# Kernel optimization log

Measured on AMD Instinct MI355X. Metric: run time of the kernel, lower is better.

## Reference

```python
import jax, jax.numpy as jnp
import numpy as np

B, N, G = 32, 1024, 8   # batch, Nvecs (= k_in), Nglobals
K_OUT, H = 128, 128     # MLP output width, hidden width
D_IN = 1 + N + G        # MLP input width: [u, norm, dots]


def setup_inputs() -> dict:
    key = jax.random.key(0)
    ks = jax.random.split(key, 8)
    x = jax.random.uniform(ks[0], (B, N, 3), dtype=jnp.float32)  # positive coords -> dots >= 0
    u = jax.random.normal(ks[1], (B, G), dtype=jnp.float32)
    s0 = 1.0 / np.sqrt(D_IN)
    s1 = 1.0 / np.sqrt(H)
    W0 = jax.random.normal(ks[2], (D_IN, H), dtype=jnp.float32) * s0
    b0 = jnp.zeros((H,), dtype=jnp.float32)
    W1 = jax.random.normal(ks[3], (H, H), dtype=jnp.float32) * s1
    b1 = jnp.zeros((H,), dtype=jnp.float32)
    W2 = jax.random.normal(ks[4], (H, K_OUT), dtype=jnp.float32) * s1
    b2 = jnp.zeros((K_OUT,), dtype=jnp.float32)
    return {"x": x, "u": u, "W0": W0, "b0": b0, "W1": W1, "b1": b1, "W2": W2, "b2": b2}


def reference(x, u, W0, b0, W1, b1, W2, b2):
    # x: [B, N, 3], u: [B, G]
    norms = jnp.linalg.norm(x, axis=-1, keepdims=True)            # [B, N, 1]
    dots = jnp.sqrt(jnp.einsum('bid,bjd->bij', x, x))             # [B, N, N]
    u_rep = jnp.broadcast_to(u[:, None, :], (x.shape[0], x.shape[1], u.shape[-1]))
    scalars = jnp.concatenate([u_rep, norms, dots], axis=-1)      # [B, N, G+1+N]
    # MLP (Linear -> LeakyReLU -> Linear -> LeakyReLU -> Linear)
    h = jax.nn.leaky_relu(scalars @ W0 + b0)
    h = jax.nn.leaky_relu(h @ W1 + b1)
    fk = h @ W2 + b2                                              # [B, N, K_OUT]
    # outer product 'bio,bid->biod' followed by mean over i == fused contraction
    out = jnp.einsum('bio,bid->bod', fk, x) / x.shape[1]          # [B, K_OUT, 3]
    return out
```

## Files before the change

### kernel.cpp

```cpp
#include <hip/hip_runtime.h>
#include <hip/hip_fp16.h>

typedef _Float16 f16;
typedef f16 f16x4 __attribute__((ext_vector_type(4)));
typedef f16 f16x8 __attribute__((ext_vector_type(8)));
typedef float f32x4 __attribute__((ext_vector_type(4)));

#define NN 1024

#define IMG_OFF   0
#define W8_OFF    327680
#define BIAS0_OFF 328192

__global__ __launch_bounds__(256) void prep_kernel(
    const float* __restrict__ u,  const float* __restrict__ W0,
    const float* __restrict__ b0, const float* __restrict__ W1,
    const float* __restrict__ W2,
    f16* __restrict__ img, float* __restrict__ w8v, float* __restrict__ bias0,
    float* __restrict__ outp)
{
    const int t = threadIdx.x;
    const int blk = blockIdx.x;
    if (blk < 160) {
        int flat = blk * 1024 + t * 4;
        int c = flat >> 13;
        int rem = flat & 8191;
        int r = rem >> 6;
        int s = rem & 63;
        int colb = s ^ ((r & 7) << 3);
        f16x4 v;
#pragma unroll
        for (int e = 0; e < 4; ++e) {
            int col = colb + e;
            float val;
            if (c < 16)       val = W0[(9 + c * 64 + col) * 128 + r];
            else if (c == 16) val = W1[col * 128 + r];
            else if (c == 17) val = W1[(64 + col) * 128 + r];
            else if (c == 18) val = W2[col * 128 + r];
            else              val = W2[(64 + col) * 128 + r];
            v[e] = (f16)val;
        }
        *(f16x4*)&img[flat] = v;
    } else if (blk < 176) {
        int idx = (blk - 160) * 256 + t;
        int b = idx >> 7, h = idx & 127;
        float s = b0[h];
#pragma unroll
        for (int g = 0; g < 8; ++g) s += u[b * 8 + g] * W0[g * 128 + h];
        bias0[idx] = s;
    } else if (blk == 176) {
        if (t < 128) w8v[t] = W0[8 * 128 + t];
    } else {
        int idx = (blk - 177) * 1024 + t * 4;
        if (idx < 12288) { float4 z = {0.f, 0.f, 0.f, 0.f}; *(float4*)&outp[idx] = z; }
    }
}

__global__ __launch_bounds__(256, 3) void fused_kernel(
    const float* __restrict__ x, const float* __restrict__ b1p,
    const float* __restrict__ b2p, const f16* __restrict__ img,
    const float* __restrict__ w8v, const float* __restrict__ bias0,
    float* __restrict__ outp)
{
    __shared__ __align__(16) f16 Dsh[2][64 * 64];
    __shared__ __align__(16) f16 Wsh[2][128 * 64];
    __shared__ __align__(16) float xi[64 * 4];
    __shared__ float normv[64];
    __shared__ float biass[128];
    __shared__ float w8s[128];

    const int t = threadIdx.x;
    const int b = blockIdx.x >> 4;
    const int i0 = (blockIdx.x & 15) * 64;

    if (t < 192) {
        int i = t / 3, d = t - i * 3;
        xi[i * 4 + d] = x[(size_t)(b * NN + i0 + i) * 3 + d];
    }
    if (t < 128) { biass[t] = bias0[b * 128 + t]; w8s[t] = w8v[t]; }
    __syncthreads();
    if (t < 64) {
        float a0 = xi[t * 4], a1 = xi[t * 4 + 1], a2 = xi[t * 4 + 2];
        normv[t] = __builtin_amdgcn_sqrtf(a0 * a0 + a1 * a1 + a2 * a2);
    }

    const int lane = t & 63, wv = t >> 6;
    const int wm = wv >> 1, wn = wv & 1;
    const int lm = lane & 15, q = lane >> 4;

    f16x4 bi[4];
#pragma unroll
    for (int it = 0; it < 4; ++it) {
        f16x4 v; v[0] = (f16)0; v[1] = (f16)0; v[2] = (f16)0; v[3] = (f16)0;
        if (q == 0) {
            int ii = it * 16 + lm;
            v[0] = (f16)xi[ii * 4];
            v[1] = (f16)xi[ii * 4 + 1];
            v[2] = (f16)xi[ii * 4 + 2];
        }
        bi[it] = v;
    }

    f16x4 aj[16];
#pragma unroll
    for (int jc = 0; jc < 16; ++jc) {
        f16x4 a; a[0] = (f16)0; a[1] = (f16)0; a[2] = (f16)0; a[3] = (f16)0;
        if (q == 0) {
            const float* p = x + (size_t)(b * NN + jc * 64 + wv * 16 + lm) * 3;
            a[0] = (f16)p[0]; a[1] = (f16)p[1]; a[2] = (f16)p[2];
        }
        aj[jc] = a;
    }

    f32x4 acc[2][4];
    auto zero_acc = [&]() {
#pragma unroll
        for (int mt = 0; mt < 2; ++mt)
#pragma unroll
            for (int nt = 0; nt < 4; ++nt)
#pragma unroll
                for (int e = 0; e < 4; ++e) acc[mt][nt][e] = 0.f;
    };
    zero_acc();

    auto stage = [&](int c, int buf) {
        const f16* g = img + c * 8192;
#pragma unroll
        for (int k = 0; k < 4; ++k) {
            int off = (t + k * 256) * 8;
            __builtin_amdgcn_global_load_lds(
                (const __attribute__((address_space(1))) unsigned int*)(g + off),
                (__attribute__((address_space(3))) unsigned int*)(&Wsh[buf][off]),
                16, 0, 0);
        }
    };

    auto dotstore = [&](f16x4 ajf, int buf) {
        f32x4 cg[4];
#pragma unroll
        for (int it = 0; it < 4; ++it) {
            f32x4 z; z[0] = 0.f; z[1] = 0.f; z[2] = 0.f; z[3] = 0.f;
            cg[it] = __builtin_amdgcn_mfma_f32_16x16x16f16(ajf, bi[it], z, 0, 0, 0);
        }
#pragma unroll
        for (int it = 0; it < 4; ++it) {
            f16x4 dv;
#pragma unroll
            for (int r = 0; r < 4; ++r)
                dv[r] = (f16)__builtin_amdgcn_sqrtf(fmaxf(cg[it][r], 0.f));
            int row = it * 16 + lm;
            int colstart = wv * 16 + q * 4;
            int addr = row * 64 + (((colstart & ~7) ^ ((row & 7) << 3)) | (colstart & 7));
            *(f16x4*)&Dsh[buf][addr] = dv;
        }
    };

    auto mfma2 = [&](const f16* Ab, const f16* Bb) {
#pragma unroll
        for (int ks = 0; ks < 2; ++ks) {
            const int col = ks * 32 + q * 8;
            f16x8 af[2], bf[4];
#pragma unroll
            for (int mt = 0; mt < 2; ++mt) {
                int row = wm * 32 + mt * 16 + lm;
                af[mt] = *(const f16x8*)(Ab + row * 64 + (col ^ ((row & 7) << 3)));
            }
#pragma unroll
            for (int nt = 0; nt < 4; ++nt) {
                int row = wn * 64 + nt * 16 + lm;
                bf[nt] = *(const f16x8*)(Bb + row * 64 + (col ^ ((row & 7) << 3)));
            }
#pragma unroll
            for (int mt = 0; mt < 2; ++mt)
#pragma unroll
                for (int nt = 0; nt < 4; ++nt)
                    acc[mt][nt] = __builtin_amdgcn_mfma_f32_16x16x32_f16(
                        af[mt], bf[nt], acc[mt][nt], 0, 0, 0);
        }
    };

    stage(0, 0);
    dotstore(aj[0], 0);
    __syncthreads();

#pragma unroll
    for (int jc = 0; jc < 16; ++jc) {
        const int cur = jc & 1, nxt = cur ^ 1;
        stage(jc + 1, nxt);
        if (jc < 15) dotstore(aj[jc + 1], nxt);
        mfma2(Dsh[cur], Wsh[cur]);
        __syncthreads();
    }

#pragma unroll
    for (int mt = 0; mt < 2; ++mt)
#pragma unroll
        for (int nt = 0; nt < 4; ++nt) {
            const int h = wn * 64 + nt * 16 + lm;
            const float bh = biass[h], w8h = w8s[h];
            const int hh = h & 63;
#pragma unroll
            for (int r = 0; r < 4; ++r) {
                int i = wm * 32 + mt * 16 + q * 4 + r;
                float val = acc[mt][nt][r] + bh + normv[i] * w8h;
                val = val > 0.f ? val : 0.01f * val;
                int addr = i * 64 + (((hh & ~7) ^ ((i & 7) << 3)) | (hh & 7));
                Dsh[wn][addr] = (f16)val;
            }
        }
    stage(17, 1);
    __syncthreads();

    zero_acc();
    mfma2(Dsh[0], Wsh[0]);
    mfma2(Dsh[1], Wsh[1]);
    __syncthreads();

#pragma unroll
    for (int mt = 0; mt < 2; ++mt)
#pragma unroll
        for (int nt = 0; nt < 4; ++nt) {
            const int h = wn * 64 + nt * 16 + lm;
            const float bh = b1p[h];
            const int hh = h & 63;
#pragma unroll
            for (int r = 0; r < 4; ++r) {
                int i = wm * 32 + mt * 16 + q * 4 + r;
                float val = acc[mt][nt][r] + bh;
                val = val > 0.f ? val : 0.01f * val;
                int addr = i * 64 + (((hh & ~7) ^ ((i & 7) << 3)) | (hh & 7));
                Dsh[wn][addr] = (f16)val;
            }
        }
    stage(18, 0);
    stage(19, 1);
    __syncthreads();

    zero_acc();
    mfma2(Dsh[0], Wsh[0]);
    mfma2(Dsh[1], Wsh[1]);

    float p[4][3];
#pragma unroll
    for (int nt = 0; nt < 4; ++nt)
#pragma unroll
        for (int d = 0; d < 3; ++d) p[nt][d] = 0.f;
    float bo[4];
#pragma unroll
    for (int nt = 0; nt < 4; ++nt) bo[nt] = b2p[wn * 64 + nt * 16 + lm];
#pragma unroll
    for (int mt = 0; mt < 2; ++mt)
#pragma unroll
        for (int r = 0; r < 4; ++r) {
            int i = wm * 32 + mt * 16 + q * 4 + r;
            float x0 = xi[i * 4], x1 = xi[i * 4 + 1], x2 = xi[i * 4 + 2];
#pragma unroll
            for (int nt = 0; nt < 4; ++nt) {
                float fkv = acc[mt][nt][r] + bo[nt];
                p[nt][0] = fmaf(fkv, x0, p[nt][0]);
                p[nt][1] = fmaf(fkv, x1, p[nt][1]);
                p[nt][2] = fmaf(fkv, x2, p[nt][2]);
            }
        }
#pragma unroll
    for (int nt = 0; nt < 4; ++nt)
#pragma unroll
        for (int d = 0; d < 3; ++d) {
            float s = p[nt][d];
            s += __shfl_xor(s, 16);
            s += __shfl_xor(s, 32);
            if (q == 0) {
                int o = wn * 64 + nt * 16 + lm;
                atomicAdd(&outp[(b * 128 + o) * 3 + d], s * (1.0f / 1024.0f));
            }
        }
}

extern "C" void kernel_launch(void* const* d_in, const int* in_sizes, int n_in,
                              void* d_out, int out_size, void* d_ws, size_t ws_size,
                              hipStream_t stream) {
    const float* x  = (const float*)d_in[0];
    const float* u  = (const float*)d_in[1];
    const float* W0 = (const float*)d_in[2];
    const float* b0 = (const float*)d_in[3];
    const float* W1 = (const float*)d_in[4];
    const float* b1 = (const float*)d_in[5];
    const float* W2 = (const float*)d_in[6];
    const float* b2 = (const float*)d_in[7];

    char* ws = (char*)d_ws;
    f16*   img   = (f16*)(ws + IMG_OFF);
    float* w8v   = (float*)(ws + W8_OFF);
    float* bias0 = (float*)(ws + BIAS0_OFF);
    float* out   = (float*)d_out;

    prep_kernel<<<189, 256, 0, stream>>>(u, W0, b0, W1, W2, img, w8v, bias0, out);
    fused_kernel<<<512, 256, 0, stream>>>(x, b1, b2, img, w8v, bias0, out);
}
```

Baseline: 96.45 us.

## Preswizzle weights into MFMA fragment layout and load directly from global

After: 93.00 us. -3.6%, faster.

```diff
diff --git a/kernel.cpp b/kernel.cpp
--- a/kernel.cpp
+++ b/kernel.cpp
@@ -8,7 +8,7 @@
 
 #define NN 1024
 
-#define IMG_OFF   0
+#define IMG2_OFF  0
 #define W8_OFF    327680
 #define BIAS0_OFF 328192
 
@@ -16,31 +16,33 @@
     const float* __restrict__ u,  const float* __restrict__ W0,
     const float* __restrict__ b0, const float* __restrict__ W1,
     const float* __restrict__ W2,
-    f16* __restrict__ img, float* __restrict__ w8v, float* __restrict__ bias0,
+    f16* __restrict__ img2, float* __restrict__ w8v, float* __restrict__ bias0,
     float* __restrict__ outp)
 {
     const int t = threadIdx.x;
     const int blk = blockIdx.x;
     if (blk < 160) {
         int flat = blk * 1024 + t * 4;
-        int c = flat >> 13;
+        int c   = flat >> 13;
         int rem = flat & 8191;
-        int r = rem >> 6;
-        int s = rem & 63;
-        int colb = s ^ ((r & 7) << 3);
+        int s0  = rem & 7;
+        int lm  = (rem >> 3) & 15;
+        int q   = (rem >> 7) & 3;
+        int ks  = (rem >> 9) & 1;
+        int nt  = (rem >> 10) & 3;
+        int wn  = (rem >> 12) & 1;
+        int n = wn * 64 + nt * 16 + lm;
         f16x4 v;
 #pragma unroll
         for (int e = 0; e < 4; ++e) {
-            int col = colb + e;
+            int k = ks * 32 + q * 8 + s0 + e;
             float val;
-            if (c < 16)       val = W0[(9 + c * 64 + col) * 128 + r];
-            else if (c == 16) val = W1[col * 128 + r];
-            else if (c == 17) val = W1[(64 + col) * 128 + r];
-            else if (c == 18) val = W2[col * 128 + r];
-            else              val = W2[(64 + col) * 128 + r];
+            if (c < 16)       val = W0[(9 + c * 64 + k) * 128 + n];
+            else if (c < 18)  val = W1[((c - 16) * 64 + k) * 128 + n];
+            else              val = W2[((c - 18) * 64 + k) * 128 + n];
             v[e] = (f16)val;
         }
-        *(f16x4*)&img[flat] = v;
+        *(f16x4*)&img2[flat] = v;
     } else if (blk < 176) {
         int idx = (blk - 160) * 256 + t;
         int b = idx >> 7, h = idx & 127;
@@ -56,14 +58,14 @@
     }
 }
 
-__global__ __launch_bounds__(256, 3) void fused_kernel(
+__global__ __launch_bounds__(256, 4) void fused_kernel(
     const float* __restrict__ x, const float* __restrict__ b1p,
-    const float* __restrict__ b2p, const f16* __restrict__ img,
+    const float* __restrict__ b2p, const f16* __restrict__ img2,
     const float* __restrict__ w8v, const float* __restrict__ bias0,
     float* __restrict__ outp)
 {
     __shared__ __align__(16) f16 Dsh[2][64 * 64];
-    __shared__ __align__(16) f16 Wsh[2][128 * 64];
+    __shared__ __align__(16) f16 xjsh[1024 * 4];
     __shared__ __align__(16) float xi[64 * 4];
     __shared__ float normv[64];
     __shared__ float biass[128];
@@ -73,6 +75,20 @@
     const int b = blockIdx.x >> 4;
     const int i0 = (blockIdx.x & 15) * 64;
 
+    {
+        const float* xb = x + (size_t)b * NN * 3;
+        float4 v0 = *(const float4*)(xb + t * 12);
+        float4 v1 = *(const float4*)(xb + t * 12 + 4);
+        float4 v2 = *(const float4*)(xb + t * 12 + 8);
+        f16x4 r0; r0[0] = (f16)v0.x; r0[1] = (f16)v0.y; r0[2] = (f16)v0.z; r0[3] = (f16)0;
+        f16x4 r1; r1[0] = (f16)v0.w; r1[1] = (f16)v1.x; r1[2] = (f16)v1.y; r1[3] = (f16)0;
+        f16x4 r2; r2[0] = (f16)v1.z; r2[1] = (f16)v1.w; r2[2] = (f16)v2.x; r2[3] = (f16)0;
+        f16x4 r3; r3[0] = (f16)v2.y; r3[1] = (f16)v2.z; r3[2] = (f16)v2.w; r3[3] = (f16)0;
+        *(f16x4*)&xjsh[(t * 4 + 0) * 4] = r0;
+        *(f16x4*)&xjsh[(t * 4 + 1) * 4] = r1;
+        *(f16x4*)&xjsh[(t * 4 + 2) * 4] = r2;
+        *(f16x4*)&xjsh[(t * 4 + 3) * 4] = r3;
+    }
     if (t < 192) {
         int i = t / 3, d = t - i * 3;
         xi[i * 4 + d] = x[(size_t)(b * NN + i0 + i) * 3 + d];
@@ -101,17 +117,6 @@
         bi[it] = v;
     }
 
-    f16x4 aj[16];
-#pragma unroll
-    for (int jc = 0; jc < 16; ++jc) {
-        f16x4 a; a[0] = (f16)0; a[1] = (f16)0; a[2] = (f16)0; a[3] = (f16)0;
-        if (q == 0) {
-            const float* p = x + (size_t)(b * NN + jc * 64 + wv * 16 + lm) * 3;
-            a[0] = (f16)p[0]; a[1] = (f16)p[1]; a[2] = (f16)p[2];
-        }
-        aj[jc] = a;
-    }
-
     f32x4 acc[2][4];
     auto zero_acc = [&]() {
 #pragma unroll
@@ -123,24 +128,15 @@
     };
     zero_acc();
 
-    auto stage = [&](int c, int buf) {
-        const f16* g = img + c * 8192;
-#pragma unroll
-        for (int k = 0; k < 4; ++k) {
-            int off = (t + k * 256) * 8;
-            __builtin_amdgcn_global_load_lds(
-                (const __attribute__((address_space(1))) unsigned int*)(g + off),
-                (__attribute__((address_space(3))) unsigned int*)(&Wsh[buf][off]),
-                16, 0, 0);
-        }
-    };
-
-    auto dotstore = [&](f16x4 ajf, int buf) {
+    auto dotstore = [&](int jc, int buf) {
+        f16x4 ajv; ajv[0] = (f16)0; ajv[1] = (f16)0; ajv[2] = (f16)0; ajv[3] = (f16)0;
+        if (q == 0)
+            ajv = *(const f16x4*)&xjsh[(jc * 64 + wv * 16 + lm) * 4];
         f32x4 cg[4];
 #pragma unroll
         for (int it = 0; it < 4; ++it) {
             f32x4 z; z[0] = 0.f; z[1] = 0.f; z[2] = 0.f; z[3] = 0.f;
-            cg[it] = __builtin_amdgcn_mfma_f32_16x16x16f16(ajf, bi[it], z, 0, 0, 0);
+            cg[it] = __builtin_amdgcn_mfma_f32_16x16x16f16(ajv, bi[it], z, 0, 0, 0);
         }
 #pragma unroll
         for (int it = 0; it < 4; ++it) {
@@ -155,40 +151,41 @@
         }
     };
 
-    auto mfma2 = [&](const f16* Ab, const f16* Bb) {
-#pragma unroll
-        for (int ks = 0; ks < 2; ++ks) {
-            const int col = ks * 32 + q * 8;
-            f16x8 af[2], bf[4];
-#pragma unroll
-            for (int mt = 0; mt < 2; ++mt) {
+    auto kstep = [&](int dbuf, int c, int dotjc, int dotbuf) {
+        f16x8 af[2][2];
+#pragma unroll
+        for (int mt = 0; mt < 2; ++mt)
+#pragma unroll
+            for (int ks = 0; ks < 2; ++ks) {
                 int row = wm * 32 + mt * 16 + lm;
-                af[mt] = *(const f16x8*)(Ab + row * 64 + (col ^ ((row & 7) << 3)));
-            }
-#pragma unroll
-            for (int nt = 0; nt < 4; ++nt) {
-                int row = wn * 64 + nt * 16 + lm;
-                bf[nt] = *(const f16x8*)(Bb + row * 64 + (col ^ ((row & 7) << 3)));
-            }
+                int col = ks * 32 + q * 8;
+                af[mt][ks] = *(const f16x8*)(Dsh[dbuf] + row * 64 + (col ^ ((row & 7) << 3)));
+            }
+        const f16* wb = img2 + (size_t)(c * 2 + wn) * 4096 + lane * 8;
+        f16x8 bf[4][2];
+#pragma unroll
+        for (int nt = 0; nt < 4; ++nt)
+#pragma unroll
+            for (int ks = 0; ks < 2; ++ks)
+                bf[nt][ks] = *(const f16x8*)(wb + (nt * 2 + ks) * 512);
+        if (dotjc >= 0) dotstore(dotjc, dotbuf);
+#pragma unroll
+        for (int ks = 0; ks < 2; ++ks)
 #pragma unroll
             for (int mt = 0; mt < 2; ++mt)
 #pragma unroll
                 for (int nt = 0; nt < 4; ++nt)
                     acc[mt][nt] = __builtin_amdgcn_mfma_f32_16x16x32_f16(
-                        af[mt], bf[nt], acc[mt][nt], 0, 0, 0);
-        }
+                        af[mt][ks], bf[nt][ks], acc[mt][nt], 0, 0, 0);
     };
 
-    stage(0, 0);
-    dotstore(aj[0], 0);
+    dotstore(0, 0);
     __syncthreads();
 
 #pragma unroll
     for (int jc = 0; jc < 16; ++jc) {
         const int cur = jc & 1, nxt = cur ^ 1;
-        stage(jc + 1, nxt);
-        if (jc < 15) dotstore(aj[jc + 1], nxt);
-        mfma2(Dsh[cur], Wsh[cur]);
+        kstep(cur, jc, (jc < 15) ? jc + 1 : -1, nxt);
         __syncthreads();
     }
 
@@ -208,12 +205,11 @@
                 Dsh[wn][addr] = (f16)val;
             }
         }
-    stage(17, 1);
     __syncthreads();
 
     zero_acc();
-    mfma2(Dsh[0], Wsh[0]);
-    mfma2(Dsh[1], Wsh[1]);
+    kstep(0, 16, -1, 0);
+    kstep(1, 17, -1, 0);
     __syncthreads();
 
 #pragma unroll
@@ -232,13 +228,11 @@
                 Dsh[wn][addr] = (f16)val;
             }
         }
-    stage(18, 0);
-    stage(19, 1);
     __syncthreads();
 
     zero_acc();
-    mfma2(Dsh[0], Wsh[0]);
-    mfma2(Dsh[1], Wsh[1]);
+    kstep(0, 18, -1, 0);
+    kstep(1, 19, -1, 0);
 
     float p[4][3];
 #pragma unroll
@@ -289,11 +283,11 @@
     const float* b2 = (const float*)d_in[7];
 
     char* ws = (char*)d_ws;
-    f16*   img   = (f16*)(ws + IMG_OFF);
+    f16*   img2  = (f16*)(ws + IMG2_OFF);
     float* w8v   = (float*)(ws + W8_OFF);
     float* bias0 = (float*)(ws + BIAS0_OFF);
     float* out   = (float*)d_out;
 
-    prep_kernel<<<189, 256, 0, stream>>>(u, W0, b0, W1, W2, img, w8v, bias0, out);
-    fused_kernel<<<512, 256, 0, stream>>>(x, b1, b2, img, w8v, bias0, out);
+    prep_kernel<<<189, 256, 0, stream>>>(u, W0, b0, W1, W2, img2, w8v, bias0, out);
+    fused_kernel<<<512, 256, 0, stream>>>(x, b1, b2, img2, w8v, bias0, out);
 }
```
